# Optimization experiments

Hardware: AMD Instinct MI355X
Metric: run time of the kernel (lower is better)

## Reference

```python
import jax, jax.numpy as jnp
import numpy as np

DIM = 4096

def _fwht_unnormalized(y):
    # y: (T, d), iterative radix-2 butterfly, unnormalized Sylvester WHT
    d = y.shape[-1]
    h = 1
    while h < d:
        y = y.reshape(-1, d // (2 * h), 2, h)
        a = y[..., 0, :]
        b = y[..., 1, :]
        y = jnp.stack([a + b, a - b], axis=-2).reshape(-1, d)
        h *= 2
    return y

def setup_inputs() -> dict:
    key = jax.random.key(0)
    x = jax.random.normal(key, (4, 2048, DIM), dtype=jnp.float32)
    return {"x": x}

def reference(x):
    # Original: x_flat @ H.T where H is built recursively with a 1/sqrt(n)
    # division at EVERY recursion level. H is symmetric, and equals the
    # unnormalized Sylvester Hadamard times 2^{-L(L+1)/4}, L = log2(d).
    shape = x.shape
    d = shape[-1]
    L = int(round(np.log2(d)))
    scale = np.float32(2.0 ** (-(L * (L + 1)) / 4.0))
    y = _fwht_unnormalized(x.reshape(-1, d))
    return (y * scale).reshape(shape)
```

## Files before the change

kernel.cpp:

```cpp
#include <hip/hip_runtime.h>


constexpr int DIM = 4096;
constexpr int PITCH = 68;

__global__ __launch_bounds__(64, 4) void fwht4096_kernel(const float* __restrict__ x,
                                                         float* __restrict__ y) {
    __shared__ float buf[32 * PITCH];
    const int lane = threadIdx.x;
    const long long row = blockIdx.x;

    float v[64];

    {
        const float4* src = reinterpret_cast<const float4*>(x + row * DIM + lane * 64);
#pragma unroll
        for (int q = 0; q < 16; ++q) {
            float4 t = src[q];
            v[4 * q + 0] = t.x;
            v[4 * q + 1] = t.y;
            v[4 * q + 2] = t.z;
            v[4 * q + 3] = t.w;
        }
    }

#pragma unroll
    for (int h = 1; h < 64; h <<= 1) {
#pragma unroll
        for (int i = 0; i < 64; i += 2 * h) {
#pragma unroll
            for (int k = 0; k < h; ++k) {
                float a = v[i + k];
                float b = v[i + k + h];
                v[i + k]     = a + b;
                v[i + k + h] = a - b;
            }
        }
    }

    float w[64];
    if (lane < 32) {
        float* wp = buf + lane * PITCH;
#pragma unroll
        for (int q = 0; q < 16; ++q) {
            float4 t = make_float4(v[4 * q], v[4 * q + 1], v[4 * q + 2], v[4 * q + 3]);
            reinterpret_cast<float4*>(wp)[q] = t;
        }
    }
    __syncthreads();
#pragma unroll
    for (int m = 0; m < 32; ++m) {
        w[m] = buf[m * PITCH + lane];
    }
    __syncthreads();

    if (lane >= 32) {
        float* wp = buf + (lane - 32) * PITCH;
#pragma unroll
        for (int q = 0; q < 16; ++q) {
            float4 t = make_float4(v[4 * q], v[4 * q + 1], v[4 * q + 2], v[4 * q + 3]);
            reinterpret_cast<float4*>(wp)[q] = t;
        }
    }
    __syncthreads();
#pragma unroll
    for (int m = 0; m < 32; ++m) {
        w[32 + m] = buf[m * PITCH + lane];
    }

#pragma unroll
    for (int h = 1; h < 64; h <<= 1) {
#pragma unroll
        for (int i = 0; i < 64; i += 2 * h) {
#pragma unroll
            for (int k = 0; k < h; ++k) {
                float a = w[i + k];
                float b = w[i + k + h];
                w[i + k]     = a + b;
                w[i + k + h] = a - b;
            }
        }
    }

    const float scale = 0x1p-39f;
    float* dst = y + row * DIM + lane;
#pragma unroll
    for (int m = 0; m < 64; ++m) {
        __builtin_nontemporal_store(w[m] * scale, dst + m * 64);
    }
}

extern "C" void kernel_launch(void* const* d_in, const int* in_sizes, int n_in,
                              void* d_out, int out_size, void* d_ws, size_t ws_size,
                              hipStream_t stream) {
    const float* x = (const float*)d_in[0];
    float* y = (float*)d_out;
    const int nrows = in_sizes[0] / DIM;
    fwht4096_kernel<<<nrows, 64, 0, stream>>>(x, y);
}
```

Measured before the change: 233.3 us.

## Use coalesced float4 loads/stores with padded LDS transpose for FWHT

Changes the per-lane data assignment so each lane loads and stores consecutive float4 chunks strided across the row, making global reads and writes fully coalesced 16-byte accesses instead of per-lane contiguous 256-byte strips and scalar strided stores. The butterfly is split into a 4-point stage within each float4 and a 16-point stage across chunks. A single padded shared-memory transpose replaces the two-phase half-wave exchange, and a second LDS round trip is added before the store so outputs leave as vector nontemporal stores. The trade is extra shared-memory traffic and syncs, plus dropping the occupancy hint from the launch bounds.

```diff
diff --git a/kernel.cpp b/kernel.cpp
--- a/kernel.cpp
+++ b/kernel.cpp
@@ -2,70 +2,71 @@
 
 
 constexpr int DIM = 4096;
-constexpr int PITCH = 68;
 
-__global__ __launch_bounds__(64, 4) void fwht4096_kernel(const float* __restrict__ x,
-                                                         float* __restrict__ y) {
-    __shared__ float buf[32 * PITCH];
+typedef float vfloat4 __attribute__((ext_vector_type(4)));
+
+__global__ __launch_bounds__(64) void fwht4096_kernel(const float* __restrict__ x,
+                                                      float* __restrict__ y) {
+    __shared__ float buf[4160];
     const int lane = threadIdx.x;
+    const int e0 = lane & 3;
+    const int g  = lane >> 2;
     const long long row = blockIdx.x;
 
     float v[64];
 
     {
-        const float4* src = reinterpret_cast<const float4*>(x + row * DIM + lane * 64);
+        const vfloat4* src = reinterpret_cast<const vfloat4*>(x + row * DIM) + lane;
 #pragma unroll
-        for (int q = 0; q < 16; ++q) {
-            float4 t = src[q];
-            v[4 * q + 0] = t.x;
-            v[4 * q + 1] = t.y;
-            v[4 * q + 2] = t.z;
-            v[4 * q + 3] = t.w;
+        for (int t = 0; t < 16; ++t) {
+            vfloat4 q = src[t * 64];
+            v[4 * t + 0] = q.x;
+            v[4 * t + 1] = q.y;
+            v[4 * t + 2] = q.z;
+            v[4 * t + 3] = q.w;
         }
     }
 
 #pragma unroll
-    for (int h = 1; h < 64; h <<= 1) {
+    for (int t = 0; t < 16; ++t) {
+        float a0 = v[4 * t + 0], a1 = v[4 * t + 1];
+        float a2 = v[4 * t + 2], a3 = v[4 * t + 3];
+        float b0 = a0 + a1, b1 = a0 - a1;
+        float b2 = a2 + a3, b3 = a2 - a3;
+        v[4 * t + 0] = b0 + b2;
+        v[4 * t + 1] = b1 + b3;
+        v[4 * t + 2] = b0 - b2;
+        v[4 * t + 3] = b1 - b3;
+    }
+
 #pragma unroll
-        for (int i = 0; i < 64; i += 2 * h) {
+    for (int h = 1; h < 16; h <<= 1) {
+#pragma unroll
+        for (int i = 0; i < 16; i += 2 * h) {
 #pragma unroll
             for (int k = 0; k < h; ++k) {
-                float a = v[i + k];
-                float b = v[i + k + h];
-                v[i + k]     = a + b;
-                v[i + k + h] = a - b;
+#pragma unroll
+                for (int e = 0; e < 4; ++e) {
+                    float a = v[4 * (i + k) + e];
+                    float b = v[4 * (i + k + h) + e];
+                    v[4 * (i + k) + e]     = a + b;
+                    v[4 * (i + k + h) + e] = a - b;
+                }
             }
         }
     }
 
-    float w[64];
-    if (lane < 32) {
-        float* wp = buf + lane * PITCH;
 #pragma unroll
-        for (int q = 0; q < 16; ++q) {
-            float4 t = make_float4(v[4 * q], v[4 * q + 1], v[4 * q + 2], v[4 * q + 3]);
-            reinterpret_cast<float4*>(wp)[q] = t;
-        }
-    }
-    __syncthreads();
-#pragma unroll
-    for (int m = 0; m < 32; ++m) {
-        w[m] = buf[m * PITCH + lane];
+    for (int t = 0; t < 16; ++t) {
+        vfloat4 q = {v[4 * t + 0], v[4 * t + 1], v[4 * t + 2], v[4 * t + 3]};
+        *reinterpret_cast<vfloat4*>(&buf[260 * t + 4 * lane]) = q;
     }
     __syncthreads();
 
-    if (lane >= 32) {
-        float* wp = buf + (lane - 32) * PITCH;
+    float w[64];
 #pragma unroll
-        for (int q = 0; q < 16; ++q) {
-            float4 t = make_float4(v[4 * q], v[4 * q + 1], v[4 * q + 2], v[4 * q + 3]);
-            reinterpret_cast<float4*>(wp)[q] = t;
-        }
-    }
-    __syncthreads();
-#pragma unroll
-    for (int m = 0; m < 32; ++m) {
-        w[32 + m] = buf[m * PITCH + lane];
+    for (int r = 0; r < 64; ++r) {
+        w[r] = buf[e0 + 4 * r + 260 * g];
     }
 
 #pragma unroll
@@ -82,11 +83,21 @@
         }
     }
 
+    __syncthreads();
+
+#pragma unroll
+    for (int r = 0; r < 64; ++r) {
+        buf[e0 + 4 * r + 260 * g] = w[r];
+    }
+    __syncthreads();
+
     const float scale = 0x1p-39f;
-    float* dst = y + row * DIM + lane;
+    vfloat4* dst = reinterpret_cast<vfloat4*>(y + row * DIM) + lane;
 #pragma unroll
-    for (int m = 0; m < 64; ++m) {
-        __builtin_nontemporal_store(w[m] * scale, dst + m * 64);
+    for (int t = 0; t < 16; ++t) {
+        vfloat4 q = *reinterpret_cast<const vfloat4*>(&buf[260 * t + 4 * lane]);
+        q *= scale;
+        __builtin_nontemporal_store(q, &dst[t * 64]);
     }
 }
 
```

After: 230.0 us. About the same (-1.4%).
